# Kernel optimization log

Hardware: AMD Instinct MI355X
Metric: run time of the kernel (lower is better)

The kernel has to match this reference:

```python
import jax, jax.numpy as jnp
import numpy as np

N = 100000      # nodes
E = 2000000     # edges
F_NODE = 32     # num_node_features
F_EDGE = 16     # num_edge_features
HID = 128       # size_conv_layers
G = 4096        # num graphs (molecules)
NCLS = 2        # class_weights.shape[0]
NEG = 0.01      # LeakyReLU default negative slope
BN_EPS = 1e-5


def _bn(h, gamma, beta):
    # torch BatchNorm1d training-mode forward: biased batch stats over node dim
    m = jnp.mean(h, axis=0)
    v = jnp.var(h, axis=0)
    return (h - m) * jax.lax.rsqrt(v + BN_EPS) * gamma + beta


def _lrelu(h):
    return jnp.where(h > 0, h, NEG * h)


def setup_inputs() -> dict:
    key = jax.random.key(0)
    ks = jax.random.split(key, 64)
    d = {}
    d["x"] = jax.random.normal(ks[0], (N, F_NODE), dtype=jnp.float32)
    d["edge_index"] = jax.random.randint(ks[1], (2, E), 0, N, dtype=jnp.int64)
    d["edge_attr"] = jax.random.normal(ks[2], (E, F_EDGE), dtype=jnp.float32)
    d["batch"] = jnp.sort(jax.random.randint(ks[3], (N,), 0, G, dtype=jnp.int64))
    dims = [F_NODE, HID, HID]  # in_channels of each conv layer
    i = 4
    for l, ic in enumerate(dims):
        d[f"eps{l}"] = jnp.zeros((), jnp.float32)                                # GINE train_eps init 0
        d[f"ew{l}"] = 0.05 * jax.random.normal(ks[i], (F_EDGE, ic), jnp.float32); i += 1
        d[f"eb{l}"] = jnp.zeros((ic,), jnp.float32)
        d[f"w1{l}"] = 0.05 * jax.random.normal(ks[i], (ic, HID), jnp.float32); i += 1
        d[f"b1{l}"] = jnp.zeros((HID,), jnp.float32)
        d[f"g1{l}"] = jnp.ones((HID,), jnp.float32)
        d[f"be1{l}"] = jnp.zeros((HID,), jnp.float32)
        d[f"w2{l}"] = 0.05 * jax.random.normal(ks[i], (HID, HID), jnp.float32); i += 1
        d[f"b2{l}"] = jnp.zeros((HID,), jnp.float32)
        d[f"g2{l}"] = jnp.ones((HID,), jnp.float32)
        d[f"be2{l}"] = jnp.zeros((HID,), jnp.float32)
    d["wf"] = 0.05 * jax.random.normal(ks[i], (2 * HID, NCLS), jnp.float32)
    d["bf"] = jnp.zeros((NCLS,), jnp.float32)
    return d


def _forward(x, edge_index, edge_attr, batch, layers, wf, bf):
    src = edge_index[0]  # x_j (messages flow source->target in PyG)
    dst = edge_index[1]  # x_i
    for (eps, ew, eb, w1, b1, g1, be1, w2, b2, g2, be2) in layers:
        e = edge_attr @ ew + eb                     # [E, in_ch]
        msg = jax.nn.relu(x[src] + e)               # GINE message
        agg = jax.ops.segment_sum(msg, dst, num_segments=N)
        h = (1.0 + eps) * x + agg                   # [N, in_ch]
        h = _lrelu(_bn(h @ w1 + b1, g1, be1))       # nn: Lin->BN->LeakyReLU
        h = h @ w2 + b2                             # nn: Lin
        x = _lrelu(_bn(h, g2, be2))                 # outer BN + LeakyReLU
    pool = jax.ops.segment_sum(x, batch, num_segments=G)  # global_add_pool
    x_cat = jnp.concatenate([x, pool[batch]], axis=1)      # repeat_interleave broadcast
    logits = x_cat @ wf + bf
    return jax.nn.softmax(logits, axis=1)


def reference(x, edge_index, edge_attr, batch,
              eps0, ew0, eb0, w10, b10, g10, be10, w20, b20, g20, be20,
              eps1, ew1, eb1, w11, b11, g11, be11, w21, b21, g21, be21,
              eps2, ew2, eb2, w12, b12, g12, be12, w22, b22, g22, be22,
              wf, bf):
    layers = [
        (eps0, ew0, eb0, w10, b10, g10, be10, w20, b20, g20, be20),
        (eps1, ew1, eb1, w11, b11, g11, be11, w21, b21, g21, be21),
        (eps2, ew2, eb2, w12, b12, g12, be12, w22, b22, g22, be22),
    ]
    return _forward(x, edge_index, edge_attr, batch, layers, wf, bf)
```

## Files before the change

### kernel.cpp

```cpp
#include <hip/hip_runtime.h>

#define GEMM_GRID 512
#define GNUM 4096

typedef __attribute__((ext_vector_type(8))) short short8_t;
typedef __attribute__((ext_vector_type(4))) float f32x4;
typedef __attribute__((ext_vector_type(2))) float v2f;

__device__ __forceinline__ float bf2f(unsigned short u) {
    union { unsigned int i; float f; } v; v.i = ((unsigned int)u) << 16; return v.f;
}
__device__ __forceinline__ unsigned short f2bf(float f) {
    union { float f; unsigned int i; } v; v.f = f;
    unsigned int b = v.i + 0x7FFFu + ((v.i >> 16) & 1u);
    return (unsigned short)(b >> 16);
}
__device__ __forceinline__ float lrelu(float v) { return v > 0.f ? v : 0.01f * v; }

__global__ __launch_bounds__(256) void hist_kernel(
    const int* __restrict__ dstv, int* __restrict__ cnt, int E)
{
    int i = blockIdx.x * 256 + threadIdx.x;
    if (i < E) atomicAdd(&cnt[dstv[i] + 1], 1);
}

__global__ __launch_bounds__(256) void scan_block_kernel(
    int* __restrict__ data, int* __restrict__ bsum, int n)
{
    __shared__ int s[256];
    int tid = threadIdx.x;
    int base = blockIdx.x * 1024 + tid * 4;
    int v[4]; int run = 0;
    #pragma unroll
    for (int i = 0; i < 4; i++) {
        int x = (base + i < n) ? data[base + i] : 0;
        run += x; v[i] = run;
    }
    s[tid] = run; __syncthreads();
    for (int off = 1; off < 256; off <<= 1) {
        int t = (tid >= off) ? s[tid - off] : 0;
        __syncthreads();
        s[tid] += t;
        __syncthreads();
    }
    int excl = s[tid] - run;
    #pragma unroll
    for (int i = 0; i < 4; i++)
        if (base + i < n) data[base + i] = v[i] + excl;
    if (tid == 255) bsum[blockIdx.x] = s[255];
}

__global__ __launch_bounds__(128) void scan_carry_kernel(int* __restrict__ bsum, int nb)
{
    __shared__ int s[128];
    int tid = threadIdx.x;
    int orig = (tid < nb) ? bsum[tid] : 0;
    s[tid] = orig; __syncthreads();
    for (int off = 1; off < 128; off <<= 1) {
        int t = (tid >= off) ? s[tid - off] : 0;
        __syncthreads();
        s[tid] += t;
        __syncthreads();
    }
    if (tid < nb) bsum[tid] = s[tid] - orig;
}

__global__ __launch_bounds__(256) void scan_add_kernel(
    int* __restrict__ data, const int* __restrict__ bsum,
    int* __restrict__ cursor, int n, int N)
{
    int i = blockIdx.x * 256 + threadIdx.x;
    if (i < n) {
        int v = data[i] + bsum[i >> 10];
        data[i] = v;
        if (i < N) cursor[i] = v;
    }
}

__global__ __launch_bounds__(256) void scatter_kernel(
    const int* __restrict__ dstv, int* __restrict__ cursor,
    int* __restrict__ perm, int E)
{
    int i = blockIdx.x * 256 + threadIdx.x;
    if (i < E) {
        int p = atomicAdd(&cursor[dstv[i]], 1);
        perm[p] = i;
    }
}

__global__ __launch_bounds__(256) void scatter_reorder_kernel(
    const int* __restrict__ dstv, const int* __restrict__ srcv,
    const float* __restrict__ ea, int* __restrict__ cursor,
    float* __restrict__ eap, int* __restrict__ srcp, int E)
{
    int i = blockIdx.x * 256 + threadIdx.x;
    if (i >= E) return;
    int p = atomicAdd(&cursor[dstv[i]], 1);
    srcp[p] = srcv[i];
    const float4* s = reinterpret_cast<const float4*>(ea) + (size_t)i * 4;
    float4* d = reinterpret_cast<float4*>(eap) + (size_t)p * 4;
    float4 v0 = s[0], v1 = s[1], v2 = s[2], v3 = s[3];
    d[0] = v0; d[1] = v1; d[2] = v2; d[3] = v3;
}

__global__ __launch_bounds__(256) void wconv_kernel(
    const float* __restrict__ w10, const float* __restrict__ w20,
    const float* __restrict__ w11, const float* __restrict__ w21,
    const float* __restrict__ w12, const float* __restrict__ w22,
    unsigned short* __restrict__ wt)
{
    int idx = blockIdx.x * 256 + threadIdx.x;
    if (idx < 4096) {
        int nn = idx >> 5, k = idx & 31;
        wt[idx] = f2bf(w10[k * 128 + nn]);
        return;
    }
    int r = idx - 4096;
    int seg = r >> 14;
    if (seg >= 5) return;
    int o = r & 16383;
    int nn = o >> 7, k = o & 127;
    const float* w = (seg == 0) ? w20 : (seg == 1) ? w11 : (seg == 2) ? w21
                   : (seg == 3) ? w12 : w22;
    wt[4096 + seg * 16384 + o] = f2bf(w[k * 128 + nn]);
    (void)nn;
}

template<bool RO>
__global__ __launch_bounds__(256) void gather_kernel32(
    const float* __restrict__ ea, const int* __restrict__ srcv,
    const int* __restrict__ perm, const int* __restrict__ off,
    const float* __restrict__ ew, const float* __restrict__ ebias,
    const float* __restrict__ epsp, const float* __restrict__ x,
    unsigned short* __restrict__ aggh, unsigned short* __restrict__ aggl, int N)
{
    __shared__ float ebuf[4][32 * 16];
    const int tid = threadIdx.x;
    const int wv = tid >> 6;
    const int lane = tid & 63;
    int n = __builtin_amdgcn_readfirstlane((int)((blockIdx.x * 256 + tid) >> 6));
    if (n >= N) return;
    const int h = lane >> 5;
    const int c = lane & 31;
    float ewr[16];
    #pragma unroll
    for (int k = 0; k < 16; k++) ewr[k] = ew[k * 32 + c];
    const float ebr = ebias[c];
    const float xself = x[(size_t)n * 32 + c];
    float acc = 0.f;
    const int p0 = off[n], end = off[n + 1];
    float* eb_ = ebuf[wv];
    const float4* eaq = reinterpret_cast<const float4*>(ea);

    for (int p = p0; p < end; p += 32) {
        int sv[16];
        #pragma unroll
        for (int j = 0; j < 16; j++) {
            int pj = min(p + h * 16 + j, end - 1);
            int e = RO ? pj : perm[pj];
            sv[j] = srcv[e];
        }
        int rowA = min(p + (lane >> 2), end - 1);
        int rowB = min(p + 16 + (lane >> 2), end - 1);
        int erA = RO ? rowA : perm[rowA];
        int erB = RO ? rowB : perm[rowB];
        float4 eaA = eaq[(size_t)erA * 4 + (lane & 3)];
        float4 eaB = eaq[(size_t)erB * 4 + (lane & 3)];
        __builtin_amdgcn_sched_barrier(0);
        float xv[16];
        #pragma unroll
        for (int j = 0; j < 16; j++)
            xv[j] = x[(size_t)sv[j] * 32 + c];
        __builtin_amdgcn_sched_barrier(0);
        __threadfence_block();
        *reinterpret_cast<float4*>(&eb_[(lane >> 2) * 16 + (lane & 3) * 4]) = eaA;
        *reinterpret_cast<float4*>(&eb_[(16 + (lane >> 2)) * 16 + (lane & 3) * 4]) = eaB;
        __threadfence_block();
        #pragma unroll
        for (int j = 0; j < 16; j++) {
            int row = h * 16 + j;
            const float4* er4 = reinterpret_cast<const float4*>(&eb_[row * 16]);
            float4 e0 = er4[0], e1 = er4[1], e2 = er4[2], e3 = er4[3];
            float u = ebr;
            u = fmaf(e0.x, ewr[0], u);  u = fmaf(e0.y, ewr[1], u);
            u = fmaf(e0.z, ewr[2], u);  u = fmaf(e0.w, ewr[3], u);
            u = fmaf(e1.x, ewr[4], u);  u = fmaf(e1.y, ewr[5], u);
            u = fmaf(e1.z, ewr[6], u);  u = fmaf(e1.w, ewr[7], u);
            u = fmaf(e2.x, ewr[8], u);  u = fmaf(e2.y, ewr[9], u);
            u = fmaf(e2.z, ewr[10], u); u = fmaf(e2.w, ewr[11], u);
            u = fmaf(e3.x, ewr[12], u); u = fmaf(e3.y, ewr[13], u);
            u = fmaf(e3.z, ewr[14], u); u = fmaf(e3.w, ewr[15], u);
            bool valid = (p + row) < end;
            acc += valid ? fmaxf(xv[j] + u, 0.f) : 0.f;
        }
    }
    acc += __shfl_xor(acc, 32);
    if (lane < 32) {
        float s = 1.f + epsp[0];
        float f = fmaf(xself, s, acc);
        unsigned int b = __float_as_uint(f);
        unsigned short hi = (unsigned short)(b >> 16);
        float lo = f - __uint_as_float(b & 0xffff0000u);
        aggh[(size_t)n * 32 + c] = hi;
        aggl[(size_t)n * 32 + c] = f2bf(lo);
    }
}

template<bool RO>
__global__ __launch_bounds__(256) void gather_kernel128_bn(
    const float* __restrict__ ea, const int* __restrict__ srcv,
    const int* __restrict__ perm, const int* __restrict__ off,
    const float* __restrict__ ew, const float* __restrict__ ebias,
    const float* __restrict__ epsp, const float* __restrict__ U,
    const float* __restrict__ stats, const float* __restrict__ g,
    const float* __restrict__ be, float invN,
    unsigned short* __restrict__ aggh, unsigned short* __restrict__ aggl, int N)
{
    int lane = threadIdx.x & 63;
    int n = __builtin_amdgcn_readfirstlane((int)((blockIdx.x * 256 + threadIdx.x) >> 6));
    if (n >= N) return;
    const int c0 = lane * 2;
    v2f scv, shv;
    {
        float m0 = stats[c0] * invN;
        float v0 = fmaxf(stats[128 + c0] * invN - m0 * m0, 0.f);
        scv.x = g[c0] * rsqrtf(v0 + 1e-5f);
        shv.x = be[c0] - m0 * scv.x;
        float m1 = stats[c0 + 1] * invN;
        float v1 = fmaxf(stats[128 + c0 + 1] * invN - m1 * m1, 0.f);
        scv.y = g[c0 + 1] * rsqrtf(v1 + 1e-5f);
        shv.y = be[c0 + 1] - m1 * scv.y;
    }
    v2f ewv[16];
    #pragma unroll
    for (int k = 0; k < 16; k++)
        ewv[k] = *reinterpret_cast<const v2f*>(&ew[k * 128 + c0]);
    const v2f ebv = *reinterpret_cast<const v2f*>(&ebias[c0]);
    const v2f xn = *reinterpret_cast<const v2f*>(&U[(size_t)n * 128 + c0]);
    v2f acc = {0.f, 0.f};
    const int p0 = off[n];
    const int end = off[n + 1];
    for (int p = p0; p < end; p += 4) {
        int ee[4]; bool vv[4];
        #pragma unroll
        for (int j = 0; j < 4; j++) {
            int pj = p + j;
            vv[j] = pj < end;
            int ij = vv[j] ? pj : p;
            ee[j] = RO ? ij : perm[ij];
        }
        int ss[4];
        #pragma unroll
        for (int j = 0; j < 4; j++) ss[j] = srcv[ee[j]];
        float4 at[4][4];
        #pragma unroll
        for (int j = 0; j < 4; j++) {
            const float4* ap = reinterpret_cast<const float4*>(ea + (size_t)ee[j] * 16);
            #pragma unroll
            for (int q = 0; q < 4; q++) at[j][q] = ap[q];
        }
        v2f xv[4];
        #pragma unroll
        for (int j = 0; j < 4; j++)
            xv[j] = *reinterpret_cast<const v2f*>(&U[(size_t)ss[j] * 128 + c0]);
        __builtin_amdgcn_sched_barrier(0);
        #pragma unroll
        for (int j = 0; j < 4; j++) {
            float av[16];
            #pragma unroll
            for (int q = 0; q < 4; q++) {
                av[4*q] = at[j][q].x; av[4*q+1] = at[j][q].y;
                av[4*q+2] = at[j][q].z; av[4*q+3] = at[j][q].w;
            }
            v2f xb = xv[j] * scv + shv;
            xb.x = lrelu(xb.x); xb.y = lrelu(xb.y);
            v2f u = ebv;
            #pragma unroll
            for (int k = 0; k < 16; k++) u = ewv[k] * av[k] + u;
            v2f m = xb + u;
            m.x = fmaxf(m.x, 0.f); m.y = fmaxf(m.y, 0.f);
            acc.x += vv[j] ? m.x : 0.f;
            acc.y += vv[j] ? m.y : 0.f;
        }
    }
    v2f xnb = xn * scv + shv;
    xnb.x = lrelu(xnb.x); xnb.y = lrelu(xnb.y);
    float s = 1.f + epsp[0];
    v2f o = xnb * s + acc;
    unsigned int b0 = __float_as_uint(o.x);
    unsigned int b1 = __float_as_uint(o.y);
    unsigned int hp = __builtin_amdgcn_perm(b1, b0, 0x07060302u);
    float l0 = o.x - __uint_as_float(b0 & 0xffff0000u);
    float l1 = o.y - __uint_as_float(b1 & 0xffff0000u);
    unsigned int lp = (unsigned int)f2bf(l0) | ((unsigned int)f2bf(l1) << 16);
    *reinterpret_cast<unsigned int*>(&aggh[(size_t)n * 128 + c0]) = hp;
    *reinterpret_cast<unsigned int*>(&aggl[(size_t)n * 128 + c0]) = lp;
}

template<int K>
__global__ __launch_bounds__(256, 3) void gemm_copy_mfma_kernel(
    const unsigned short* __restrict__ Ah, const unsigned short* __restrict__ Al,
    const unsigned short* __restrict__ Wpre, const float* __restrict__ bias,
    float* __restrict__ out, float* __restrict__ stats_out, int N, int ntiles)
{
    constexpr int PA = K + 8;
    __shared__ unsigned short As_hi[32 * PA];
    __shared__ unsigned short As_lo[32 * PA];
    __shared__ unsigned short Wt[128 * PA];
    const int tid = threadIdx.x;
    const int w = tid >> 6;
    const int lane = tid & 63;
    const int quad = lane >> 4;
    const int l16 = lane & 15;
    const int rbase = (w & 1) * 16;
    const int nbase = (w >> 1) * 4;

    constexpr int C8 = K / 8;
    for (int idx = tid; idx < 128 * C8; idx += 256) {
        int nn = idx / C8, c8 = idx % C8;
        *reinterpret_cast<uint4*>(&Wt[nn * PA + c8 * 8]) =
            *reinterpret_cast<const uint4*>(&Wpre[nn * K + c8 * 8]);
    }
    float bcol[4];
    #pragma unroll
    for (int nt = 0; nt < 4; nt++) bcol[nt] = bias[(nbase + nt) * 16 + l16];
    float csum[4] = {0.f, 0.f, 0.f, 0.f}, csq[4] = {0.f, 0.f, 0.f, 0.f};

    for (int tile = blockIdx.x; tile < ntiles; tile += gridDim.x) {
        const int row0 = tile * 32;
        __syncthreads();
        for (int cid = tid; cid < 32 * C8; cid += 256) {
            int row = cid / C8, c8 = cid % C8;
            int r = row0 + row;
            uint4 h, l;
            if (r < N) {
                h = *reinterpret_cast<const uint4*>(&Ah[(size_t)r * K + c8 * 8]);
                l = *reinterpret_cast<const uint4*>(&Al[(size_t)r * K + c8 * 8]);
            } else {
                h = make_uint4(0u,0u,0u,0u);
                l = make_uint4(0u,0u,0u,0u);
            }
            *reinterpret_cast<uint4*>(&As_hi[row * PA + c8 * 8]) = h;
            *reinterpret_cast<uint4*>(&As_lo[row * PA + c8 * 8]) = l;
        }
        __syncthreads();

        f32x4 acc[4];
        #pragma unroll
        for (int nt = 0; nt < 4; nt++) { f32x4 z = {0.f,0.f,0.f,0.f}; acc[nt] = z; }
        #pragma unroll
        for (int chunk = 0; chunk < K / 32; chunk++) {
            short8_t ahi = *reinterpret_cast<const short8_t*>(
                &As_hi[(rbase + l16) * PA + chunk * 32 + quad * 8]);
            short8_t alo = *reinterpret_cast<const short8_t*>(
                &As_lo[(rbase + l16) * PA + chunk * 32 + quad * 8]);
            #pragma unroll
            for (int nt = 0; nt < 4; nt++) {
                short8_t bfr = *reinterpret_cast<const short8_t*>(
                    &Wt[((nbase + nt) * 16 + l16) * PA + chunk * 32 + quad * 8]);
                acc[nt] = __builtin_amdgcn_mfma_f32_16x16x32_bf16(alo, bfr, acc[nt], 0, 0, 0);
                acc[nt] = __builtin_amdgcn_mfma_f32_16x16x32_bf16(ahi, bfr, acc[nt], 0, 0, 0);
            }
        }
        const int rb = row0 + rbase + quad * 4;
        #pragma unroll
        for (int nt = 0; nt < 4; nt++) {
            #pragma unroll
            for (int rg = 0; rg < 4; rg++) {
                int r = rb + rg;
                if (r < N) {
                    float v = acc[nt][rg] + bcol[nt];
                    out[(size_t)r * 128 + (nbase + nt) * 16 + l16] = v;
                    csum[nt] += v; csq[nt] += v * v;
                }
            }
        }
    }
    #pragma unroll
    for (int nt = 0; nt < 4; nt++) {
        float s = csum[nt]; s += __shfl_xor(s, 16); s += __shfl_xor(s, 32);
        float q = csq[nt];  q += __shfl_xor(q, 16); q += __shfl_xor(q, 32);
        if (quad == 0) {
            int col = (nbase + nt) * 16 + l16;
            atomicAdd(&stats_out[col], s);
            atomicAdd(&stats_out[128 + col], q);
        }
    }
}

__global__ __launch_bounds__(256, 3) void gemm_bn_mfma_kernel(
    const float* __restrict__ A,
    const float* __restrict__ stats_in, const float* __restrict__ g,
    const float* __restrict__ be, float invN,
    const unsigned short* __restrict__ Wpre, const float* __restrict__ bias,
    float* __restrict__ out, float* __restrict__ stats_out, int N, int ntiles)
{
    constexpr int K = 128;
    constexpr int PA = K + 8;
    __shared__ unsigned short As_hi[32 * PA];
    __shared__ unsigned short As_lo[32 * PA];
    __shared__ unsigned short Wt[128 * PA];
    __shared__ float scale_s[K];
    __shared__ float shift_s[K];
    const int tid = threadIdx.x;
    const int w = tid >> 6;
    const int lane = tid & 63;
    const int quad = lane >> 4;
    const int l16 = lane & 15;
    const int rbase = (w & 1) * 16;
    const int nbase = (w >> 1) * 4;

    constexpr int C8 = K / 8;
    for (int idx = tid; idx < 128 * C8; idx += 256) {
        int nn = idx / C8, c8 = idx % C8;
        *reinterpret_cast<uint4*>(&Wt[nn * PA + c8 * 8]) =
            *reinterpret_cast<const uint4*>(&Wpre[nn * K + c8 * 8]);
    }
    for (int i = tid; i < K; i += 256) {
        float m = stats_in[i] * invN;
        float va = fmaxf(stats_in[K + i] * invN - m * m, 0.f);
        float sc = g[i] * rsqrtf(va + 1e-5f);
        scale_s[i] = sc;
        shift_s[i] = be[i] - m * sc;
    }
    float bcol[4];
    #pragma unroll
    for (int nt = 0; nt < 4; nt++) bcol[nt] = bias[(nbase + nt) * 16 + l16];
    float csum[4] = {0.f, 0.f, 0.f, 0.f}, csq[4] = {0.f, 0.f, 0.f, 0.f};

    for (int tile = blockIdx.x; tile < ntiles; tile += gridDim.x) {
        const int row0 = tile * 32;
        __syncthreads();
        for (int cid = tid; cid < 32 * C8; cid += 256) {
            int row = cid / C8, c8 = cid % C8;
            int r = row0 + row;
            float f[8];
            if (r < N) {
                float4 u0 = *reinterpret_cast<const float4*>(&A[(size_t)r * K + c8 * 8]);
                float4 u1 = *reinterpret_cast<const float4*>(&A[(size_t)r * K + c8 * 8 + 4]);
                f[0]=u0.x; f[1]=u0.y; f[2]=u0.z; f[3]=u0.w;
                f[4]=u1.x; f[5]=u1.y; f[6]=u1.z; f[7]=u1.w;
            } else {
                #pragma unroll
                for (int j = 0; j < 8; j++) f[j] = 0.f;
            }
            int kb = c8 * 8;
            #pragma unroll
            for (int j = 0; j < 8; j++)
                f[j] = lrelu(fmaf(f[j], scale_s[kb + j], shift_s[kb + j]));
            unsigned int hi[4], lo[4];
            #pragma unroll
            for (int j = 0; j < 4; j++) {
                unsigned int b0 = __float_as_uint(f[2*j]);
                unsigned int b1 = __float_as_uint(f[2*j + 1]);
                hi[j] = __builtin_amdgcn_perm(b1, b0, 0x07060302u);
                float l0 = f[2*j]     - __uint_as_float(b0 & 0xffff0000u);
                float l1 = f[2*j + 1] - __uint_as_float(b1 & 0xffff0000u);
                lo[j] = __builtin_amdgcn_perm(__float_as_uint(l1), __float_as_uint(l0), 0x07060302u);
            }
            *reinterpret_cast<uint4*>(&As_hi[row * PA + c8 * 8]) = make_uint4(hi[0], hi[1], hi[2], hi[3]);
            *reinterpret_cast<uint4*>(&As_lo[row * PA + c8 * 8]) = make_uint4(lo[0], lo[1], lo[2], lo[3]);
        }
        __syncthreads();

        f32x4 acc[4];
        #pragma unroll
        for (int nt = 0; nt < 4; nt++) { f32x4 z = {0.f,0.f,0.f,0.f}; acc[nt] = z; }
        #pragma unroll
        for (int chunk = 0; chunk < K / 32; chunk++) {
            short8_t ahi = *reinterpret_cast<const short8_t*>(
                &As_hi[(rbase + l16) * PA + chunk * 32 + quad * 8]);
            short8_t alo = *reinterpret_cast<const short8_t*>(
                &As_lo[(rbase + l16) * PA + chunk * 32 + quad * 8]);
            #pragma unroll
            for (int nt = 0; nt < 4; nt++) {
                short8_t bfr = *reinterpret_cast<const short8_t*>(
                    &Wt[((nbase + nt) * 16 + l16) * PA + chunk * 32 + quad * 8]);
                acc[nt] = __builtin_amdgcn_mfma_f32_16x16x32_bf16(alo, bfr, acc[nt], 0, 0, 0);
                acc[nt] = __builtin_amdgcn_mfma_f32_16x16x32_bf16(ahi, bfr, acc[nt], 0, 0, 0);
            }
        }
        const int rb = row0 + rbase + quad * 4;
        #pragma unroll
        for (int nt = 0; nt < 4; nt++) {
            #pragma unroll
            for (int rg = 0; rg < 4; rg++) {
                int r = rb + rg;
                if (r < N) {
                    float v = acc[nt][rg] + bcol[nt];
                    out[(size_t)r * 128 + (nbase + nt) * 16 + l16] = v;
                    csum[nt] += v; csq[nt] += v * v;
                }
            }
        }
    }
    #pragma unroll
    for (int nt = 0; nt < 4; nt++) {
        float s = csum[nt]; s += __shfl_xor(s, 16); s += __shfl_xor(s, 32);
        float q = csq[nt];  q += __shfl_xor(q, 16); q += __shfl_xor(q, 32);
        if (quad == 0) {
            int col = (nbase + nt) * 16 + l16;
            atomicAdd(&stats_out[col], s);
            atomicAdd(&stats_out[128 + col], q);
        }
    }
}

__global__ __launch_bounds__(256) void pool_kernel_bn(
    const float* __restrict__ U, const int* __restrict__ batch,
    const float* __restrict__ stats, const float* __restrict__ g,
    const float* __restrict__ be, float invN,
    float* __restrict__ pool, int N)
{
    int w = (blockIdx.x * 256 + threadIdx.x) >> 6;
    int lane = threadIdx.x & 63;
    int n0 = w * 32;
    if (n0 >= N) return;
    int n1 = min(n0 + 32, N);
    int c0 = lane * 2;
    float sc0, sh0, sc1, sh1;
    {
        float m0 = stats[c0] * invN;
        float v0 = fmaxf(stats[128 + c0] * invN - m0 * m0, 0.f);
        sc0 = g[c0] * rsqrtf(v0 + 1e-5f);
        sh0 = be[c0] - m0 * sc0;
        float m1 = stats[c0 + 1] * invN;
        float v1 = fmaxf(stats[128 + c0 + 1] * invN - m1 * m1, 0.f);
        sc1 = g[c0 + 1] * rsqrtf(v1 + 1e-5f);
        sh1 = be[c0 + 1] - m1 * sc1;
    }
    float a0 = 0.f, a1 = 0.f;
    int cur = batch[n0];
    for (int n = n0; n < n1; ++n) {
        int b = batch[n];
        if (b != cur) {
            atomicAdd(&pool[(size_t)cur * 128 + c0], a0);
            atomicAdd(&pool[(size_t)cur * 128 + c0 + 1], a1);
            a0 = a1 = 0.f; cur = b;
        }
        float2 v = *reinterpret_cast<const float2*>(&U[(size_t)n * 128 + c0]);
        a0 += lrelu(fmaf(v.x, sc0, sh0));
        a1 += lrelu(fmaf(v.y, sc1, sh1));
    }
    atomicAdd(&pool[(size_t)cur * 128 + c0], a0);
    atomicAdd(&pool[(size_t)cur * 128 + c0 + 1], a1);
}

__global__ __launch_bounds__(256) void final_kernel_bn(
    const float* __restrict__ U, const float* __restrict__ pool,
    const int* __restrict__ batch,
    const float* __restrict__ stats, const float* __restrict__ g,
    const float* __restrict__ be, float invN,
    const float* __restrict__ wf, const float* __restrict__ bf,
    float* __restrict__ out, int N)
{
    __shared__ float wf_s[512];
    int tid = threadIdx.x;
    for (int i = tid; i < 512; i += 256) wf_s[i] = wf[i];
    __syncthreads();
    int wid = tid >> 6, lane = tid & 63;
    int n = blockIdx.x * 4 + wid;
    if (n >= N) return;
    int cA = lane, cB = 64 + lane;
    float scA, shA, scB, shB;
    {
        float mA = stats[cA] * invN;
        float vA = fmaxf(stats[128 + cA] * invN - mA * mA, 0.f);
        scA = g[cA] * rsqrtf(vA + 1e-5f);
        shA = be[cA] - mA * scA;
        float mB = stats[cB] * invN;
        float vB = fmaxf(stats[128 + cB] * invN - mB * mB, 0.f);
        scB = g[cB] * rsqrtf(vB + 1e-5f);
        shB = be[cB] - mB * scB;
    }
    int b = batch[n];
    float v0 = lrelu(fmaf(U[(size_t)n * 128 + cA], scA, shA));
    float v1 = lrelu(fmaf(U[(size_t)n * 128 + cB], scB, shB));
    float p0 = pool[(size_t)b * 128 + cA];
    float p1 = pool[(size_t)b * 128 + cB];
    float a0 = v0 * wf_s[lane * 2]       + v1 * wf_s[(64 + lane) * 2]
             + p0 * wf_s[(128 + lane) * 2] + p1 * wf_s[(192 + lane) * 2];
    float a1 = v0 * wf_s[lane * 2 + 1]       + v1 * wf_s[(64 + lane) * 2 + 1]
             + p0 * wf_s[(128 + lane) * 2 + 1] + p1 * wf_s[(192 + lane) * 2 + 1];
    #pragma unroll
    for (int off = 32; off >= 1; off >>= 1) {
        a0 += __shfl_down(a0, off);
        a1 += __shfl_down(a1, off);
    }
    if (lane == 0) {
        a0 += bf[0]; a1 += bf[1];
        float mx = fmaxf(a0, a1);
        float e0 = __expf(a0 - mx), e1 = __expf(a1 - mx);
        float inv = 1.f / (e0 + e1);
        out[(size_t)n * 2]     = e0 * inv;
        out[(size_t)n * 2 + 1] = e1 * inv;
    }
}

extern "C" void kernel_launch(void* const* d_in, const int* in_sizes, int n_in,
                              void* d_out, int out_size, void* d_ws, size_t ws_size,
                              hipStream_t stream)
{
    const float* x0    = (const float*)d_in[0];
    const int*   ei    = (const int*)d_in[1];
    const float* ea    = (const float*)d_in[2];
    const int*   batch = (const int*)d_in[3];
    const int E = in_sizes[1] / 2;
    const int N = in_sizes[3];
    const int* srcv = ei;
    const int* dstv = ei + E;
    const float* wf = (const float*)d_in[37];
    const float* bfp = (const float*)d_in[38];
    float* out = (float*)d_out;
    const float invN = 1.0f / (float)N;
    const int ntiles = (N + 31) / 32;

    const size_t base_f = (size_t)2 * N * 128 + (size_t)GNUM * 128 + 6 * 256
                        + (size_t)(N + 1) + (size_t)N + 128 + (size_t)E;
    const size_t full_f = base_f + (size_t)E * 16 + (size_t)E;
    const bool ro = (ws_size >= full_f * 4);

    float* ws = (float*)d_ws;
    size_t o = 0;
    float* xA    = ws + o; o += (size_t)N * 128;
    float* xB    = ws + o; o += (size_t)N * 128;
    float* eap   = ws + o; o += ro ? (size_t)E * 16 : 0;
    float* poolb = ws + o; o += (size_t)GNUM * 128;
    float* statsb= ws + o; o += 6 * 256;
    int* srcp    = (int*)(ws + o); o += ro ? (size_t)E : 0;
    int* off     = (int*)(ws + o); o += (size_t)(N + 1);
    int* cursor  = (int*)(ws + o); o += (size_t)N;
    int* bsumb   = (int*)(ws + o); o += 128;
    int* perm    = (int*)(ws + o);

    unsigned short* planeh = (unsigned short*)xB;
    unsigned short* wtbuf = (unsigned short*)cursor;

    hipMemsetAsync(off, 0, (size_t)(N + 1) * sizeof(int), stream);
    hipMemsetAsync(statsb, 0, (size_t)6 * 256 * sizeof(float), stream);
    hipMemsetAsync(poolb, 0, (size_t)GNUM * 128 * sizeof(float), stream);
    hist_kernel<<<(E + 255) / 256, 256, 0, stream>>>(dstv, off, E);
    const int n1 = N + 1;
    const int nb = (n1 + 1023) / 1024;
    scan_block_kernel<<<nb, 256, 0, stream>>>(off, bsumb, n1);
    scan_carry_kernel<<<1, 128, 0, stream>>>(bsumb, nb);
    scan_add_kernel<<<(n1 + 255) / 256, 256, 0, stream>>>(off, bsumb, cursor, n1, N);
    if (ro)
        scatter_reorder_kernel<<<(E + 255) / 256, 256, 0, stream>>>(
            dstv, srcv, ea, cursor, eap, srcp, E);
    else
        scatter_kernel<<<(E + 255) / 256, 256, 0, stream>>>(dstv, cursor, perm, E);

    wconv_kernel<<<(86016 + 255) / 256, 256, 0, stream>>>(
        (const float*)d_in[4 + 3], (const float*)d_in[4 + 7],
        (const float*)d_in[15 + 3], (const float*)d_in[15 + 7],
        (const float*)d_in[26 + 3], (const float*)d_in[26 + 7], wtbuf);
    const unsigned short* w1p[3] = { wtbuf, wtbuf + 4096 + 16384,
                                     wtbuf + 4096 + 3 * 16384 };
    const unsigned short* w2p[3] = { wtbuf + 4096, wtbuf + 4096 + 2 * 16384,
                                     wtbuf + 4096 + 4 * 16384 };

    const float* g_ea  = ro ? eap  : ea;
    const int*   g_src = ro ? srcp : srcv;
    const int gather_blocks = (N + 3) / 4;

    const float *pg = nullptr, *pbe = nullptr;
    float* pstats = nullptr;

    for (int l = 0; l < 3; l++) {
        const int C = (l == 0) ? 32 : 128;
        int bidx = 4 + l * 11;
        const float* epsp = (const float*)d_in[bidx + 0];
        const float* ew   = (const float*)d_in[bidx + 1];
        const float* eb   = (const float*)d_in[bidx + 2];
        const float* b1   = (const float*)d_in[bidx + 4];
        const float* g1   = (const float*)d_in[bidx + 5];
        const float* be1  = (const float*)d_in[bidx + 6];
        const float* b2   = (const float*)d_in[bidx + 8];
        const float* g2   = (const float*)d_in[bidx + 9];
        const float* be2  = (const float*)d_in[bidx + 10];
        float* st1 = statsb + (size_t)(l * 2) * 256;
        float* st2 = statsb + (size_t)(l * 2 + 1) * 256;

        unsigned short* ah = planeh;
        unsigned short* al = planeh + (size_t)N * C;

        if (l == 0) {
            if (ro) gather_kernel32<true><<<gather_blocks, 256, 0, stream>>>(
                        g_ea, g_src, perm, off, ew, eb, epsp, x0, ah, al, N);
            else    gather_kernel32<false><<<gather_blocks, 256, 0, stream>>>(
                        g_ea, g_src, perm, off, ew, eb, epsp, x0, ah, al, N);
            gemm_copy_mfma_kernel<32><<<GEMM_GRID, 256, 0, stream>>>(
                ah, al, w1p[0], b1, xA, st1, N, ntiles);
        } else {
            if (ro) gather_kernel128_bn<true><<<gather_blocks, 256, 0, stream>>>(
                        g_ea, g_src, perm, off, ew, eb, epsp, xA,
                        pstats, pg, pbe, invN, ah, al, N);
            else    gather_kernel128_bn<false><<<gather_blocks, 256, 0, stream>>>(
                        g_ea, g_src, perm, off, ew, eb, epsp, xA,
                        pstats, pg, pbe, invN, ah, al, N);
            gemm_copy_mfma_kernel<128><<<GEMM_GRID, 256, 0, stream>>>(
                ah, al, w1p[l], b1, xA, st1, N, ntiles);
        }
        gemm_bn_mfma_kernel<<<GEMM_GRID, 256, 0, stream>>>(
            xA, st1, g1, be1, invN, w2p[l], b2, xA, st2, N, ntiles);
        pstats = st2; pg = g2; pbe = be2;
    }
    pool_kernel_bn<<<((N + 31) / 32 * 64 + 255) / 256, 256, 0, stream>>>(
        xA, batch, pstats, pg, pbe, invN, poolb, N);
    final_kernel_bn<<<(N + 3) / 4, 256, 0, stream>>>(
        xA, poolb, batch, pstats, pg, pbe, invN, wf, bfp, out, N);
}
```

Measured before the change: 1.234 ms.

## Precompute BN+LeakyReLU node features in bf16 before 128-channel gather

Adds a pass that applies the previous layer's BatchNorm and LeakyReLU once per node and stores the result as bf16. The 128-channel gather then reads these 4-byte bf16 pairs instead of fp32 values, and no longer recomputes BN per neighbor. This halves the bytes fetched in the random neighbor gathers, at the cost of an extra kernel pass and lower precision on gathered activations. It also clamps tail indices instead of using p, and the fallback path drops its template.

```diff
diff --git a/kernel.cpp b/kernel.cpp
--- a/kernel.cpp
+++ b/kernel.cpp
@@ -124,6 +124,42 @@
                    : (seg == 3) ? w12 : w22;
     wt[4096 + seg * 16384 + o] = f2bf(w[k * 128 + nn]);
     (void)nn;
+}
+
+__global__ __launch_bounds__(256) void bnact_kernel(
+    const float* __restrict__ U, const float* __restrict__ stats,
+    const float* __restrict__ g, const float* __restrict__ be, float invN,
+    unsigned short* __restrict__ B, int N)
+{
+    int idx = blockIdx.x * 256 + threadIdx.x;
+    if (idx >= N * 16) return;
+    int n = idx >> 4;
+    int c8 = (idx & 15) * 8;
+    float4 u0 = *reinterpret_cast<const float4*>(&U[(size_t)n * 128 + c8]);
+    float4 u1 = *reinterpret_cast<const float4*>(&U[(size_t)n * 128 + c8 + 4]);
+    float f[8] = {u0.x, u0.y, u0.z, u0.w, u1.x, u1.y, u1.z, u1.w};
+    unsigned int pk[4];
+    #pragma unroll
+    for (int j = 0; j < 4; j++) {
+        unsigned short r0, r1;
+        {
+            int c = c8 + 2 * j;
+            float m = stats[c] * invN;
+            float v = fmaxf(stats[128 + c] * invN - m * m, 0.f);
+            float sc = g[c] * rsqrtf(v + 1e-5f);
+            r0 = f2bf(lrelu(fmaf(f[2*j], sc, be[c] - m * sc)));
+        }
+        {
+            int c = c8 + 2 * j + 1;
+            float m = stats[c] * invN;
+            float v = fmaxf(stats[128 + c] * invN - m * m, 0.f);
+            float sc = g[c] * rsqrtf(v + 1e-5f);
+            r1 = f2bf(lrelu(fmaf(f[2*j+1], sc, be[c] - m * sc)));
+        }
+        pk[j] = (unsigned int)r0 | ((unsigned int)r1 << 16);
+    }
+    *reinterpret_cast<uint4*>(&B[(size_t)n * 128 + c8]) =
+        make_uint4(pk[0], pk[1], pk[2], pk[3]);
 }
 
 template<bool RO>
@@ -206,7 +242,83 @@
     }
 }
 
-template<bool RO>
+__global__ __launch_bounds__(256) void gather_kernel128_b(
+    const float* __restrict__ ea, const int* __restrict__ srcv,
+    const int* __restrict__ off,
+    const float* __restrict__ ew, const float* __restrict__ ebias,
+    const float* __restrict__ epsp, const unsigned short* __restrict__ B,
+    unsigned short* __restrict__ aggh, unsigned short* __restrict__ aggl, int N)
+{
+    int lane = threadIdx.x & 63;
+    int n = __builtin_amdgcn_readfirstlane((int)((blockIdx.x * 256 + threadIdx.x) >> 6));
+    if (n >= N) return;
+    const int c0 = lane * 2;
+    v2f ewv[16];
+    #pragma unroll
+    for (int k = 0; k < 16; k++)
+        ewv[k] = *reinterpret_cast<const v2f*>(&ew[k * 128 + c0]);
+    const v2f ebv = *reinterpret_cast<const v2f*>(&ebias[c0]);
+    unsigned int bs = *reinterpret_cast<const unsigned int*>(&B[(size_t)n * 128 + c0]);
+    v2f xnb;
+    xnb.x = __uint_as_float(bs << 16);
+    xnb.y = __uint_as_float(bs & 0xffff0000u);
+    v2f acc = {0.f, 0.f};
+    const int p0 = off[n];
+    const int end = off[n + 1];
+    const int endm1 = end - 1;
+    for (int p = p0; p < end; p += 4) {
+        int ss[4]; bool vv[4];
+        #pragma unroll
+        for (int j = 0; j < 4; j++) {
+            int pj = p + j;
+            vv[j] = pj < end;
+            ss[j] = srcv[min(pj, endm1)];
+        }
+        float4 at[4][4];
+        #pragma unroll
+        for (int j = 0; j < 4; j++) {
+            const float4* ap = reinterpret_cast<const float4*>(
+                ea + (size_t)min(p + j, endm1) * 16);
+            #pragma unroll
+            for (int q = 0; q < 4; q++) at[j][q] = ap[q];
+        }
+        unsigned int xb[4];
+        #pragma unroll
+        for (int j = 0; j < 4; j++)
+            xb[j] = *reinterpret_cast<const unsigned int*>(&B[(size_t)ss[j] * 128 + c0]);
+        __builtin_amdgcn_sched_barrier(0);
+        #pragma unroll
+        for (int j = 0; j < 4; j++) {
+            float av[16];
+            #pragma unroll
+            for (int q = 0; q < 4; q++) {
+                av[4*q] = at[j][q].x; av[4*q+1] = at[j][q].y;
+                av[4*q+2] = at[j][q].z; av[4*q+3] = at[j][q].w;
+            }
+            v2f xv;
+            xv.x = __uint_as_float(xb[j] << 16);
+            xv.y = __uint_as_float(xb[j] & 0xffff0000u);
+            v2f u = ebv;
+            #pragma unroll
+            for (int k = 0; k < 16; k++) u = ewv[k] * av[k] + u;
+            v2f m = xv + u;
+            m.x = fmaxf(m.x, 0.f); m.y = fmaxf(m.y, 0.f);
+            acc.x += vv[j] ? m.x : 0.f;
+            acc.y += vv[j] ? m.y : 0.f;
+        }
+    }
+    float s = 1.f + epsp[0];
+    v2f o = xnb * s + acc;
+    unsigned int b0 = __float_as_uint(o.x);
+    unsigned int b1 = __float_as_uint(o.y);
+    unsigned int hp = __builtin_amdgcn_perm(b1, b0, 0x07060302u);
+    float l0 = o.x - __uint_as_float(b0 & 0xffff0000u);
+    float l1 = o.y - __uint_as_float(b1 & 0xffff0000u);
+    unsigned int lp = (unsigned int)f2bf(l0) | ((unsigned int)f2bf(l1) << 16);
+    *reinterpret_cast<unsigned int*>(&aggh[(size_t)n * 128 + c0]) = hp;
+    *reinterpret_cast<unsigned int*>(&aggl[(size_t)n * 128 + c0]) = lp;
+}
+
 __global__ __launch_bounds__(256) void gather_kernel128_bn(
     const float* __restrict__ ea, const int* __restrict__ srcv,
     const int* __restrict__ perm, const int* __restrict__ off,
@@ -247,7 +359,7 @@
             int pj = p + j;
             vv[j] = pj < end;
             int ij = vv[j] ? pj : p;
-            ee[j] = RO ? ij : perm[ij];
+            ee[j] = perm[ij];
         }
         int ss[4];
         #pragma unroll
@@ -617,7 +729,7 @@
 
     const size_t base_f = (size_t)2 * N * 128 + (size_t)GNUM * 128 + 6 * 256
                         + (size_t)(N + 1) + (size_t)N + 128 + (size_t)E;
-    const size_t full_f = base_f + (size_t)E * 16 + (size_t)E;
+    const size_t full_f = base_f + (size_t)E * 16 + (size_t)E + (size_t)N * 64;
     const bool ro = (ws_size >= full_f * 4);
 
     float* ws = (float*)d_ws;
@@ -625,6 +737,7 @@
     float* xA    = ws + o; o += (size_t)N * 128;
     float* xB    = ws + o; o += (size_t)N * 128;
     float* eap   = ws + o; o += ro ? (size_t)E * 16 : 0;
+    float* bnbf  = ws + o; o += ro ? (size_t)N * 64 : 0;
     float* poolb = ws + o; o += (size_t)GNUM * 128;
     float* statsb= ws + o; o += 6 * 256;
     int* srcp    = (int*)(ws + o); o += ro ? (size_t)E : 0;
@@ -634,6 +747,7 @@
     int* perm    = (int*)(ws + o);
 
     unsigned short* planeh = (unsigned short*)xB;
+    unsigned short* bnb = (unsigned short*)bnbf;
     unsigned short* wtbuf = (unsigned short*)cursor;
 
     hipMemsetAsync(off, 0, (size_t)(N + 1) * sizeof(int), stream);
@@ -668,7 +782,6 @@
     float* pstats = nullptr;
 
     for (int l = 0; l < 3; l++) {
-        const int C = (l == 0) ? 32 : 128;
         int bidx = 4 + l * 11;
         const float* epsp = (const float*)d_in[bidx + 0];
         const float* ew   = (const float*)d_in[bidx + 1];
@@ -683,7 +796,7 @@
         float* st2 = statsb + (size_t)(l * 2 + 1) * 256;
 
         unsigned short* ah = planeh;
-        unsigned short* al = planeh + (size_t)N * C;
+        unsigned short* al = planeh + (size_t)N * ((l == 0) ? 32 : 128);
 
         if (l == 0) {
             if (ro) gather_kernel32<true><<<gather_blocks, 256, 0, stream>>>(
@@ -693,12 +806,16 @@
             gemm_copy_mfma_kernel<32><<<GEMM_GRID, 256, 0, stream>>>(
                 ah, al, w1p[0], b1, xA, st1, N, ntiles);
         } else {
-            if (ro) gather_kernel128_bn<true><<<gather_blocks, 256, 0, stream>>>(
-                        g_ea, g_src, perm, off, ew, eb, epsp, xA,
-                        pstats, pg, pbe, invN, ah, al, N);
-            else    gather_kernel128_bn<false><<<gather_blocks, 256, 0, stream>>>(
-                        g_ea, g_src, perm, off, ew, eb, epsp, xA,
-                        pstats, pg, pbe, invN, ah, al, N);
+            if (ro) {
+                bnact_kernel<<<(N * 16 + 255) / 256, 256, 0, stream>>>(
+                    xA, pstats, pg, pbe, invN, bnb, N);
+                gather_kernel128_b<<<gather_blocks, 256, 0, stream>>>(
+                    g_ea, g_src, off, ew, eb, epsp, bnb, ah, al, N);
+            } else {
+                gather_kernel128_bn<<<gather_blocks, 256, 0, stream>>>(
+                    g_ea, g_src, perm, off, ew, eb, epsp, xA,
+                    pstats, pg, pbe, invN, ah, al, N);
+            }
             gemm_copy_mfma_kernel<128><<<GEMM_GRID, 256, 0, stream>>>(
                 ah, al, w1p[l], b1, xA, st1, N, ntiles);
         }
```

After: 1.220 ms. About the same (-1.1%).
